# Kernel optimization log

Measured on AMD Instinct MI355X. Metric: run time of the kernel, lower is better.

Reference implementation:

```python
import jax, jax.numpy as jnp
import numpy as np

B, S, D = 2, 2048, 4096
NH, NKV = 32, 8
HD = D // NH  # 128
N_REP = NH // NKV  # 4


def setup_inputs() -> dict:
    key = jax.random.key(0)
    ks = jax.random.split(key, 5)
    scale = 0.02
    return {
        "x": jax.random.normal(ks[0], (B, S, D), dtype=jnp.float32),
        "wq": jax.random.normal(ks[1], (D, NH * HD), dtype=jnp.float32) * scale,
        "wk": jax.random.normal(ks[2], (D, NKV * HD), dtype=jnp.float32) * scale,
        "wv": jax.random.normal(ks[3], (D, NKV * HD), dtype=jnp.float32) * scale,
        "wo": jax.random.normal(ks[4], (NH * HD, D), dtype=jnp.float32) * scale,
    }


def reference(x, wq, wk, wv, wo):
    bsz, toks, _ = x.shape
    q = (x @ wq).reshape(bsz, toks, NH, HD)      # [B,S,NH,HD]
    k = (x @ wk).reshape(bsz, toks, NKV, HD)     # [B,S,NKV,HD]
    v = (x @ wv).reshape(bsz, toks, NKV, HD)
    # GQA: fold n_rep into einsum instead of materializing repeated K/V.
    qg = q.reshape(bsz, toks, NKV, N_REP, HD)    # group query heads per kv head
    scores = jnp.einsum('bqgrd,bkgd->bgrqk', qg, k) / jnp.sqrt(jnp.asarray(HD, x.dtype))
    attn = jax.nn.softmax(scores.astype(jnp.float32), axis=-1).astype(x.dtype)
    out = jnp.einsum('bgrqk,bkgd->bqgrd', attn, v)  # [B,S,NKV,N_REP,HD]
    out = out.reshape(bsz, toks, NH * HD)
    return out @ wo
```

## Files before the change

### kernel.cpp

```cpp
#include <hip/hip_runtime.h>
#include <math.h>

typedef _Float16 f16;
using f16x8 = __attribute__((ext_vector_type(8))) _Float16;
using f32x4 = __attribute__((ext_vector_type(4))) float;

#define BATCH 2
#define SEQ   2048
#define DMODEL 4096
#define NH    32
#define NKV   8
#define HD    128
#define MTOK  (BATCH*SEQ)

__global__ __launch_bounds__(256) void prep1_k(const float* __restrict__ x, f16* __restrict__ xh,
                                               const float* __restrict__ wq, f16* __restrict__ wqT,
                                               float scale) {
  __shared__ float tile[32][33];
  const int bid = blockIdx.x, t = threadIdx.x;
  if (bid < 8192) {
    const int i = bid * 256 + t;
    const float4* p = reinterpret_cast<const float4*>(x) + (size_t)i * 2;
    float4 a = p[0], b = p[1];
    f16x8 o = { (f16)a.x, (f16)a.y, (f16)a.z, (f16)a.w,
                (f16)b.x, (f16)b.y, (f16)b.z, (f16)b.w };
    reinterpret_cast<f16x8*>(xh)[i] = o;
  } else {
    const int bb = bid - 8192;
    const int n0 = (bb & 127) * 32, k0 = (bb >> 7) * 32;
    const int r = t >> 3, c4 = (t & 7) << 2;
    const float4 v = *reinterpret_cast<const float4*>(wq + (size_t)(k0 + r) * DMODEL + n0 + c4);
    tile[r][c4 + 0] = v.x; tile[r][c4 + 1] = v.y; tile[r][c4 + 2] = v.z; tile[r][c4 + 3] = v.w;
    __syncthreads();
    union { f16 h[4]; ushort4 u4; } pk;
    pk.h[0] = (f16)(tile[c4 + 0][r] * scale);
    pk.h[1] = (f16)(tile[c4 + 1][r] * scale);
    pk.h[2] = (f16)(tile[c4 + 2][r] * scale);
    pk.h[3] = (f16)(tile[c4 + 3][r] * scale);
    *reinterpret_cast<ushort4*>(wqT + (size_t)(n0 + r) * DMODEL + k0 + c4) = pk.u4;
  }
}

__global__ __launch_bounds__(256) void transpose_cvt_k(const float* __restrict__ w,
                                                       f16* __restrict__ wt, int Kd, int Nd,
                                                       float scale) {
  __shared__ float tile[32][33];
  const int t = threadIdx.x;
  const int n0 = blockIdx.x * 32, k0 = blockIdx.y * 32;
  const int r = t >> 3, c4 = (t & 7) << 2;
  const float4 v = *reinterpret_cast<const float4*>(w + (size_t)(k0 + r) * Nd + n0 + c4);
  tile[r][c4 + 0] = v.x; tile[r][c4 + 1] = v.y; tile[r][c4 + 2] = v.z; tile[r][c4 + 3] = v.w;
  __syncthreads();
  union { f16 h[4]; ushort4 u4; } pk;
  pk.h[0] = (f16)(tile[c4 + 0][r] * scale);
  pk.h[1] = (f16)(tile[c4 + 1][r] * scale);
  pk.h[2] = (f16)(tile[c4 + 2][r] * scale);
  pk.h[3] = (f16)(tile[c4 + 3][r] * scale);
  *reinterpret_cast<ushort4*>(wt + (size_t)(n0 + r) * Kd + k0 + c4) = pk.u4;
}

__global__ __launch_bounds__(256) void transpose_cvt2_k(const float* __restrict__ w0,
                                                        const float* __restrict__ w1,
                                                        f16* __restrict__ wt, int Kd, int Nd) {
  __shared__ float tile[32][33];
  const float* w = blockIdx.z ? w1 : w0;
  f16* dst = wt + (size_t)blockIdx.z * Nd * Kd;
  const int t = threadIdx.x;
  const int n0 = blockIdx.x * 32, k0 = blockIdx.y * 32;
  const int r = t >> 3, c4 = (t & 7) << 2;
  const float4 v = *reinterpret_cast<const float4*>(w + (size_t)(k0 + r) * Nd + n0 + c4);
  tile[r][c4 + 0] = v.x; tile[r][c4 + 1] = v.y; tile[r][c4 + 2] = v.z; tile[r][c4 + 3] = v.w;
  __syncthreads();
  union { f16 h[4]; ushort4 u4; } pk;
  pk.h[0] = (f16)tile[c4 + 0][r];
  pk.h[1] = (f16)tile[c4 + 1][r];
  pk.h[2] = (f16)tile[c4 + 2][r];
  pk.h[3] = (f16)tile[c4 + 3][r];
  *reinterpret_cast<ushort4*>(dst + (size_t)(n0 + r) * Kd + k0 + c4) = pk.u4;
}

__global__ __launch_bounds__(512, 2) void gemm_kv8_k(const f16* __restrict__ A,
                                                     const f16* __restrict__ BT,
                                                     f16* __restrict__ Kc,
                                                     f16* __restrict__ Vt,
                                                     int M, int N, int K) {
  __shared__ f16 lds[2 * 24576];
  char* ldsb = (char*)lds;

  const int t = threadIdx.x, lane = t & 63, w = t >> 6;
  const int wm = w >> 2, wn = w & 3;
  const int ll = lane & 15, lg = lane >> 4;
  const int nbn = N >> 8;
  const int nwg = gridDim.x, cpx = nwg >> 3, bid = blockIdx.x;
  const int swz = (bid & 7) * cpx + (bid >> 3);
  const int bm = swz / nbn, bn = swz % nbn;
  const size_t m0 = (size_t)bm << 7, n0 = (size_t)bn << 8;
  const int NT = K >> 6;

  const int uoff[4] = {0, 8192, 16384, 32768};

  auto stage = [&](int bufI, int unit, int ktS) {
    char* dstb = ldsb + (size_t)bufI * 49152 + uoff[unit];
    if (unit < 2) {
      const f16* base = A + (m0 + (size_t)(unit & 1) * 64) * (size_t)K;
      const int row = t >> 3, lin = t & 7;
      const int slot = lin ^ (row & 7);
      const f16* src = base + (size_t)row * K + ktS + slot * 8;
      __builtin_amdgcn_global_load_lds((const __attribute__((address_space(1))) void*)src,
          (__attribute__((address_space(3))) void*)(dstb + (size_t)t * 16), 16, 0, 0);
    } else {
      const f16* base = BT + (n0 + (size_t)(unit & 1) * 128) * (size_t)K;
#pragma unroll
      for (int rr = 0; rr < 2; rr++) {
        const int u = t + rr * 512;
        const int row = u >> 3, lin = u & 7;
        const int slot = lin ^ (row & 7);
        const f16* src = base + (size_t)row * K + ktS + slot * 8;
        __builtin_amdgcn_global_load_lds((const __attribute__((address_space(1))) void*)src,
            (__attribute__((address_space(3))) void*)(dstb + (size_t)u * 16), 16, 0, 0);
      }
    }
  };

  f32x4 acc[4][4];
#pragma unroll
  for (int i = 0; i < 4; i++)
#pragma unroll
    for (int j = 0; j < 4; j++) acc[i][j] = f32x4{0.f, 0.f, 0.f, 0.f};

  f16x8 af[2][2];
  f16x8 bfr[2][2][2];

  stage(0, 0, 0); stage(0, 1, 0); stage(0, 2, 0); stage(0, 3, 0);
  stage(1, 0, 64); stage(1, 2, 64); stage(1, 3, 64);
  asm volatile("s_waitcnt vmcnt(5)" ::: "memory");
  __builtin_amdgcn_sched_barrier(0);
  __builtin_amdgcn_s_barrier();

#define PHK(RBUF, RDA, RDB, SBUF, SUNIT, STILE, VM, MH, NHQ) do {                         \
    if ((RDA) >= 0) {                                                                     \
      const char* ab = ldsb + (size_t)(RBUF) * 49152 + uoff[MH];                          \
      _Pragma("unroll") for (int mi2 = 0; mi2 < 2; mi2++)                                 \
        _Pragma("unroll") for (int kk = 0; kk < 2; kk++) {                                \
          const int ri = wm * 32 + mi2 * 16 + ll;                                         \
          af[mi2][kk] = *reinterpret_cast<const f16x8*>(ab + ri * 128                     \
                               + ((((kk << 2) + lg) ^ (ri & 7)) << 4));                   \
        }                                                                                 \
    }                                                                                     \
    if ((RDB) >= 0) {                                                                     \
      const char* bb = ldsb + (size_t)(RBUF) * 49152 + uoff[2 + (RDB)];                   \
      _Pragma("unroll") for (int ni2 = 0; ni2 < 2; ni2++)                                 \
        _Pragma("unroll") for (int kk = 0; kk < 2; kk++) {                                \
          const int ri = wn * 32 + ni2 * 16 + ll;                                         \
          bfr[RDB][ni2][kk] = *reinterpret_cast<const f16x8*>(bb + ri * 128               \
                               + ((((kk << 2) + lg) ^ (ri & 7)) << 4));                   \
        }                                                                                 \
    }                                                                                     \
    stage((SBUF), (SUNIT), ((STILE) & (NT - 1)) << 6);                                    \
    if (VM) { asm volatile("s_waitcnt vmcnt(5)" ::: "memory");                            \
              __builtin_amdgcn_sched_barrier(0); }                                        \
    __builtin_amdgcn_s_barrier();                                                         \
    asm volatile("s_waitcnt lgkmcnt(0)" ::: "memory");                                    \
    __builtin_amdgcn_sched_barrier(0);                                                    \
    __builtin_amdgcn_s_setprio(1);                                                        \
    _Pragma("unroll") for (int kk = 0; kk < 2; kk++)                                      \
      _Pragma("unroll") for (int mi2 = 0; mi2 < 2; mi2++)                                 \
        _Pragma("unroll") for (int ni2 = 0; ni2 < 2; ni2++)                               \
          acc[(MH) * 2 + mi2][(NHQ) * 2 + ni2] = __builtin_amdgcn_mfma_f32_16x16x32_f16(  \
              af[mi2][kk], bfr[NHQ][ni2][kk], acc[(MH) * 2 + mi2][(NHQ) * 2 + ni2],       \
              0, 0, 0);                                                                   \
    __builtin_amdgcn_s_setprio(0);                                                        \
    __builtin_amdgcn_s_barrier();                                                         \
  } while (0)

  for (int tt = 0; tt < NT; tt += 2) {
    PHK(0,  0,  0, 1, 1, tt + 1, false, 0, 0);
    PHK(0, -1,  1, 0, 0, tt + 2, false, 0, 1);
    PHK(0,  1, -1, 0, 2, tt + 2, false, 1, 0);
    PHK(0, -1, -1, 0, 3, tt + 2, true , 1, 1);
    PHK(1,  0,  0, 0, 1, tt + 2, false, 0, 0);
    PHK(1, -1,  1, 1, 0, tt + 3, false, 0, 1);
    PHK(1,  1, -1, 1, 2, tt + 3, false, 1, 0);
    PHK(1, -1, -1, 1, 3, tt + 3, true , 1, 1);
  }
#undef PHK

#pragma unroll
  for (int mh = 0; mh < 2; mh++)
#pragma unroll
    for (int mi2 = 0; mi2 < 2; mi2++) {
      const size_t r0 = m0 + mh * 64 + wm * 32 + mi2 * 16 + lg * 4;
#pragma unroll
      for (int nh = 0; nh < 2; nh++)
#pragma unroll
        for (int ni2 = 0; ni2 < 2; ni2++) {
          const size_t c = n0 + nh * 128 + wn * 32 + ni2 * 16 + ll;
          const f32x4 v = acc[mh * 2 + mi2][nh * 2 + ni2];
          if ((int)c < 1024) {
#pragma unroll
            for (int rr = 0; rr < 4; rr++) Kc[(r0 + rr) * 1024 + c] = (f16)v[rr];
          } else {
            const int nc = (int)c - 1024;
            const int kvh = nc >> 7, d = nc & 127;
            const int b = (int)(r0 >> 11), sc = (int)(r0 & 2047);
            union { f16 h[4]; ushort4 u4; } pk;
#pragma unroll
            for (int rr = 0; rr < 4; rr++) pk.h[rr] = (f16)v[rr];
            *reinterpret_cast<ushort4*>(Vt + (((size_t)(b * NKV + kvh) * HD + d) * SEQ + sc)) = pk.u4;
          }
        }
    }
}

template<int MODE>
__global__ __launch_bounds__(512, 2) void gemm256_k(const f16* __restrict__ A,
                                                    const f16* __restrict__ BT,
                                                    void* __restrict__ Cv,
                                                    int M, int N, int K) {
  __shared__ f16 lds[2 * 4 * 128 * 64];
  char* ldsb = (char*)lds;

  const int t = threadIdx.x, lane = t & 63, w = t >> 6;
  const int wm = w >> 2, wn = w & 3;
  const int ll = lane & 15, lg = lane >> 4;
  const int nbn = N >> 8;
  const int nwg = gridDim.x, cpx = nwg >> 3, bid = blockIdx.x;
  const int swz = (bid & 7) * cpx + (bid >> 3);
  const int bm = swz / nbn, bn = swz % nbn;
  const size_t m0 = (size_t)bm << 8, n0 = (size_t)bn << 8;
  const int NT = K >> 6;

  auto stage = [&](int bufI, int unit, int ktS) {
    const f16* base = (unit < 2) ? (A + (m0 + (size_t)(unit & 1) * 128) * (size_t)K)
                                 : (BT + (n0 + (size_t)(unit & 1) * 128) * (size_t)K);
#pragma unroll
    for (int rr = 0; rr < 2; rr++) {
      const int u = t + rr * 512;
      const int row = u >> 3, lin = u & 7;
      const int slot = lin ^ (row & 7);
      const f16* src = base + (size_t)row * K + ktS + slot * 8;
      char* dst = ldsb + (size_t)(bufI * 4 + unit) * 16384 + (size_t)(w * 64 + rr * 512) * 16;
      __builtin_amdgcn_global_load_lds((const __attribute__((address_space(1))) void*)src,
          (__attribute__((address_space(3))) void*)dst, 16, 0, 0);
    }
  };

  f32x4 acc[8][4];
#pragma unroll
  for (int i = 0; i < 8; i++)
#pragma unroll
    for (int j = 0; j < 4; j++) acc[i][j] = f32x4{0.f, 0.f, 0.f, 0.f};

  f16x8 af[4][2];
  f16x8 bfr[2][2][2];

  stage(0, 0, 0); stage(0, 2, 0); stage(0, 3, 0); stage(0, 1, 0);
  stage(1, 0, 64); stage(1, 2, 64); stage(1, 3, 64);
  asm volatile("s_waitcnt vmcnt(6)" ::: "memory");
  __builtin_amdgcn_sched_barrier(0);
  __builtin_amdgcn_s_barrier();

#define PH(RBUF, RDA, RDB, SBUF, SUNIT, STILE, VM, MH, NHQ) do {                          \
    if ((RDA) >= 0) {                                                                     \
      const char* ab = ldsb + (size_t)((RBUF) * 4 + (RDA)) * 16384;                       \
      _Pragma("unroll") for (int mi = 0; mi < 4; mi++)                                    \
        _Pragma("unroll") for (int kk = 0; kk < 2; kk++)                                  \
          af[mi][kk] = *reinterpret_cast<const f16x8*>(ab + (mi * 32 + wm * 16 + ll) * 128\
                               + ((((kk << 2) + lg) ^ (ll & 7)) << 4));                   \
    }                                                                                     \
    if ((RDB) >= 0) {                                                                     \
      const char* bb = ldsb + (size_t)((RBUF) * 4 + 2 + (RDB)) * 16384;                   \
      _Pragma("unroll") for (int ni = 0; ni < 2; ni++)                                    \
        _Pragma("unroll") for (int kk = 0; kk < 2; kk++)                                  \
          bfr[RDB][ni][kk] = *reinterpret_cast<const f16x8*>(bb +                         \
                               (wn * 32 + ni * 16 + ll) * 128                             \
                               + ((((kk << 2) + lg) ^ (ll & 7)) << 4));                   \
    }                                                                                     \
    stage((SBUF), (SUNIT), ((STILE) & (NT - 1)) << 6);                                    \
    if (VM) { asm volatile("s_waitcnt vmcnt(6)" ::: "memory");                            \
              __builtin_amdgcn_sched_barrier(0); }                                        \
    __builtin_amdgcn_s_barrier();                                                         \
    asm volatile("s_waitcnt lgkmcnt(0)" ::: "memory");                                    \
    __builtin_amdgcn_sched_barrier(0);                                                    \
    __builtin_amdgcn_s_setprio(1);                                                        \
    _Pragma("unroll") for (int kk = 0; kk < 2; kk++)                                      \
      _Pragma("unroll") for (int mi = 0; mi < 4; mi++)                                    \
        _Pragma("unroll") for (int ni = 0; ni < 2; ni++)                                  \
          acc[(MH) * 4 + mi][(NHQ) * 2 + ni] = __builtin_amdgcn_mfma_f32_16x16x32_f16(    \
              af[mi][kk], bfr[NHQ][ni][kk], acc[(MH) * 4 + mi][(NHQ) * 2 + ni], 0, 0, 0); \
    __builtin_amdgcn_s_setprio(0);                                                        \
    __builtin_amdgcn_s_barrier();                                                         \
  } while (0)

  for (int tt = 0; tt < NT; tt += 2) {
    PH(0,  0,  0, 1, 1, tt + 1, false, 0, 0);
    PH(0, -1,  1, 0, 0, tt + 2, false, 0, 1);
    PH(0,  1, -1, 0, 2, tt + 2, false, 1, 0);
    PH(0, -1, -1, 0, 3, tt + 2, true , 1, 1);
    PH(1,  0,  0, 0, 1, tt + 2, false, 0, 0);
    PH(1, -1,  1, 1, 0, tt + 3, false, 0, 1);
    PH(1,  1, -1, 1, 2, tt + 3, false, 1, 0);
    PH(1, -1, -1, 1, 3, tt + 3, true , 1, 1);
  }
#undef PH

#pragma unroll
  for (int mh = 0; mh < 2; mh++)
#pragma unroll
    for (int mi = 0; mi < 4; mi++) {
      const size_t r0 = m0 + mh * 128 + mi * 32 + wm * 16 + lg * 4;
#pragma unroll
      for (int nh = 0; nh < 2; nh++)
#pragma unroll
        for (int ni = 0; ni < 2; ni++) {
          const size_t c = n0 + nh * 128 + wn * 32 + ni * 16 + ll;
          const f32x4 v = acc[mh * 4 + mi][nh * 2 + ni];
          if (MODE == 0) {
            f16* C = (f16*)Cv;
#pragma unroll
            for (int rr = 0; rr < 4; rr++) C[(r0 + rr) * N + c] = (f16)v[rr];
          } else {
            float* C = (float*)Cv;
#pragma unroll
            for (int rr = 0; rr < 4; rr++) C[(r0 + rr) * N + c] = v[rr];
          }
        }
    }
}

__global__ __launch_bounds__(512) void attn_k10(const f16* __restrict__ Q,
                                                const f16* __restrict__ Kb,
                                                const f16* __restrict__ VT,
                                                f16* __restrict__ ctx) {
  __shared__ f16 Klds[2][64 * 128];
  __shared__ f16 Vlds[2][128 * 64];
  __shared__ f16 Plds[8][16 * 64];

  const int t = threadIdx.x, lane = t & 63, w = t >> 6;
  const int bid = blockIdx.x;
  const int swz = (bid & 7) * 128 + (bid >> 3);
  const int qt = swz & 63, kvh = (swz >> 6) & 7, b = swz >> 9;
  const int h = kvh * 4 + (w & 3);
  const int q0 = qt * 32 + (w >> 2) * 16;
  const int ll = lane & 15, lg = lane >> 4;

  const f16* Qb = Q + ((size_t)(b * SEQ + q0) * NH + h) * HD;
  const f16* Kh = Kb + ((size_t)b * SEQ * NKV + kvh) * HD;
  const f16* Vh = VT + ((size_t)(b * NKV + kvh)) * HD * SEQ;

  f16x8 qf[4];
#pragma unroll
  for (int kd = 0; kd < 4; kd++)
    qf[kd] = *reinterpret_cast<const f16x8*>(Qb + (size_t)ll * (NH * HD) + kd * 32 + lg * 8);

  float m_ = -INFINITY;
  float l_ = 0.f;
  f32x4 o[8];
#pragma unroll
  for (int df = 0; df < 8; df++) o[df] = f32x4{0.f, 0.f, 0.f, 0.f};

  const float THR = 11.5416f;

  auto stage = [&](int bufi, int kt) {
#pragma unroll
    for (int rr = 0; rr < 2; rr++) {
      const int u = w * 128 + rr * 64 + lane;
      const int krow = u >> 4, klin = u & 15;
      const int kslot = klin ^ (krow & 7);
      const f16* ksrc = Kh + (size_t)(kt + krow) * (NKV * HD) + kslot * 8;
      __builtin_amdgcn_global_load_lds((const __attribute__((address_space(1))) void*)ksrc,
          (__attribute__((address_space(3))) void*)((char*)&Klds[bufi][0] + (size_t)u * 16), 16, 0, 0);
      const int vrow = u >> 3, vlin = u & 7;
      const int vslot = vlin ^ (vrow & 7);
      const f16* vsrc = Vh + (size_t)vrow * SEQ + kt + vslot * 8;
      __builtin_amdgcn_global_load_lds((const __attribute__((address_space(1))) void*)vsrc,
          (__attribute__((address_space(3))) void*)((char*)&Vlds[bufi][0] + (size_t)u * 16), 16, 0, 0);
    }
  };

  stage(0, 0);
  __syncthreads();

  for (int kt = 0; kt < SEQ; kt += 64) {
    const int buf = (kt >> 6) & 1;
    if (kt + 64 < SEQ) stage(buf ^ 1, kt + 64);

    const char* Kt = (const char*)Klds[buf];
    const char* Vt = (const char*)Vlds[buf];

    f32x4 s[4];
    __builtin_amdgcn_s_setprio(1);
#pragma unroll
    for (int nf = 0; nf < 4; nf++) {
      f32x4 a = f32x4{0.f, 0.f, 0.f, 0.f};
#pragma unroll
      for (int kd = 0; kd < 4; kd++) {
        const int row = nf * 16 + ll;
        f16x8 kf = *reinterpret_cast<const f16x8*>(
            Kt + row * 256 + ((((kd << 2) + lg) ^ (row & 7)) << 4));
        a = __builtin_amdgcn_mfma_f32_16x16x32_f16(kf, qf[kd], a, 0, 0, 0);
      }
      s[nf] = a;
    }
    __builtin_amdgcn_s_setprio(0);

    float mx = s[0][0];
#pragma unroll
    for (int nf = 0; nf < 4; nf++)
#pragma unroll
      for (int r = 0; r < 4; r++) mx = fmaxf(mx, s[nf][r]);

    if (!__all((int)(mx <= m_ + THR))) {
      float mr = fmaxf(mx, __shfl_xor(mx, 16, 64));
      mr = fmaxf(mr, __shfl_xor(mr, 32, 64));
      const float mn = fmaxf(m_, mr);
      const float corrq = __builtin_amdgcn_exp2f(m_ - mn);
      m_ = mn;
      l_ *= corrq;
#pragma unroll
      for (int r = 0; r < 4; r++) {
        const float c = __shfl(corrq, (lane & 48) | (lg * 4 + r), 64);
#pragma unroll
        for (int df = 0; df < 8; df++) o[df][r] *= c;
      }
    }

    float rs = 0.f;
#pragma unroll
    for (int nf = 0; nf < 4; nf++)
#pragma unroll
      for (int r = 0; r < 4; r++) {
        const float p = __builtin_amdgcn_exp2f(s[nf][r] - m_);
        s[nf][r] = p;
        rs += p;
      }
    rs += __shfl_xor(rs, 16, 64);
    rs += __shfl_xor(rs, 32, 64);
    l_ += rs;

    char* Pw = (char*)&Plds[w][0];
#pragma unroll
    for (int nf = 0; nf < 4; nf++) {
      union { f16 h[4]; ushort4 u4; } pk;
#pragma unroll
      for (int r = 0; r < 4; r++) pk.h[r] = (f16)s[nf][r];
      *reinterpret_cast<ushort4*>(Pw + ll * 128 + ((nf * 32 + lg * 8) ^ ((ll & 7) << 4))) = pk.u4;
    }

    f16x8 pf[2];
#pragma unroll
    for (int kf = 0; kf < 2; kf++)
      pf[kf] = *reinterpret_cast<const f16x8*>(Pw + ll * 128 + (((kf << 6) + (lg << 4)) ^ ((ll & 7) << 4)));

    __builtin_amdgcn_s_setprio(1);
#pragma unroll
    for (int kf = 0; kf < 2; kf++)
#pragma unroll
      for (int df = 0; df < 8; df++) {
        const int row = df * 16 + ll;
        f16x8 vf = *reinterpret_cast<const f16x8*>(
            Vt + row * 128 + ((((kf << 2) + lg) ^ (row & 7)) << 4));
        o[df] = __builtin_amdgcn_mfma_f32_16x16x32_f16(pf[kf], vf, o[df], 0, 0, 0);
      }
    __builtin_amdgcn_s_setprio(0);

    __syncthreads();
  }

  float inv[4];
#pragma unroll
  for (int r = 0; r < 4; r++) {
    const float lq = __shfl(l_, (lane & 48) | (lg * 4 + r), 64);
    inv[r] = 1.0f / lq;
  }
  f16* cb = ctx + ((size_t)(b * SEQ + q0) * NH + h) * HD;
#pragma unroll
  for (int df = 0; df < 8; df++)
#pragma unroll
    for (int r = 0; r < 4; r++)
      cb[(size_t)(lg * 4 + r) * (NH * HD) + df * 16 + ll] = (f16)(o[df][r] * inv[r]);
}

extern "C" void kernel_launch(void* const* d_in, const int* in_sizes, int n_in,
                              void* d_out, int out_size, void* d_ws, size_t ws_size,
                              hipStream_t stream) {
  (void)in_sizes; (void)n_in; (void)out_size;
  const float* x  = (const float*)d_in[0];
  const float* wq = (const float*)d_in[1];
  const float* wk = (const float*)d_in[2];
  const float* wv = (const float*)d_in[3];
  const float* wo = (const float*)d_in[4];
  float* out = (float*)d_out;

  const size_t SZ_X  = (size_t)MTOK * DMODEL * sizeof(f16);
  const size_t SZ_KV = (size_t)MTOK * NKV * HD * sizeof(f16);
  if (ws_size < 3 * SZ_X + 2 * SZ_KV) return;

  char* ws = (char*)d_ws;
  f16* xh  = (f16*)ws;
  f16* wT  = (f16*)(ws + SZ_X);
  f16* Qb  = (f16*)(ws + 2 * SZ_X);
  f16* Kb  = (f16*)(ws + 3 * SZ_X);
  f16* VTb = (f16*)(ws + 3 * SZ_X + SZ_KV);

  const float KSC2 = 0.08838834764831845f * 1.4426950408889634f;

  prep1_k<<<dim3(8192 + 16384), 256, 0, stream>>>(x, xh, wq, wT, KSC2);
  gemm256_k<0><<<dim3((MTOK / 256) * (DMODEL / 256)), 512, 0, stream>>>(xh, wT, Qb, MTOK, DMODEL, DMODEL);

  transpose_cvt2_k<<<dim3(NKV * HD / 32, DMODEL / 32, 2), 256, 0, stream>>>(wk, wv, wT, DMODEL, NKV * HD);
  gemm_kv8_k<<<dim3((MTOK / 128) * (2048 / 256)), 512, 0, stream>>>(xh, wT, Kb, VTb, MTOK, 2048, DMODEL);

  attn_k10<<<dim3(BATCH * NKV * (SEQ / 32)), 512, 0, stream>>>(Qb, Kb, VTb, xh);

  transpose_cvt_k<<<dim3(DMODEL / 32, DMODEL / 32), 256, 0, stream>>>(wo, wT, DMODEL, DMODEL, 1.0f);
  gemm256_k<2><<<dim3((MTOK / 256) * (DMODEL / 256)), 512, 0, stream>>>(xh, wT, out, MTOK, DMODEL, DMODEL);
}
```

Before: 526.3 us.

## Fuse all weight transposes into a single prep kernel with separate buffers

All weight conversion and transpose work (wq, wk, wv and optionally wo) now runs in one large prep launch, writing into separate workspace buffers when enough workspace is available. This removes three extra launches and the serial small transpose kernels between GEMMs. A fallback path keeps the old sequence when workspace is small. The gemm256 phase macro also gains a partial lgkmcnt wait before the barrier. The cost is extra workspace memory.

```diff
diff --git a/kernel.cpp b/kernel.cpp
--- a/kernel.cpp
+++ b/kernel.cpp
@@ -13,9 +13,12 @@
 #define HD    128
 #define MTOK  (BATCH*SEQ)
 
-__global__ __launch_bounds__(256) void prep1_k(const float* __restrict__ x, f16* __restrict__ xh,
-                                               const float* __restrict__ wq, f16* __restrict__ wqT,
-                                               float scale) {
+__global__ __launch_bounds__(256) void prep_k(const float* __restrict__ x, f16* __restrict__ xh,
+                                              const float* __restrict__ wq, f16* __restrict__ wqT,
+                                              const float* __restrict__ wk, const float* __restrict__ wv,
+                                              f16* __restrict__ wkvT,
+                                              const float* __restrict__ wo, f16* __restrict__ woT,
+                                              float scale) {
   __shared__ float tile[32][33];
   const int bid = blockIdx.x, t = threadIdx.x;
   if (bid < 8192) {
@@ -25,20 +28,26 @@
     f16x8 o = { (f16)a.x, (f16)a.y, (f16)a.z, (f16)a.w,
                 (f16)b.x, (f16)b.y, (f16)b.z, (f16)b.w };
     reinterpret_cast<f16x8*>(xh)[i] = o;
-  } else {
-    const int bb = bid - 8192;
-    const int n0 = (bb & 127) * 32, k0 = (bb >> 7) * 32;
-    const int r = t >> 3, c4 = (t & 7) << 2;
-    const float4 v = *reinterpret_cast<const float4*>(wq + (size_t)(k0 + r) * DMODEL + n0 + c4);
-    tile[r][c4 + 0] = v.x; tile[r][c4 + 1] = v.y; tile[r][c4 + 2] = v.z; tile[r][c4 + 3] = v.w;
-    __syncthreads();
-    union { f16 h[4]; ushort4 u4; } pk;
-    pk.h[0] = (f16)(tile[c4 + 0][r] * scale);
-    pk.h[1] = (f16)(tile[c4 + 1][r] * scale);
-    pk.h[2] = (f16)(tile[c4 + 2][r] * scale);
-    pk.h[3] = (f16)(tile[c4 + 3][r] * scale);
-    *reinterpret_cast<ushort4*>(wqT + (size_t)(n0 + r) * DMODEL + k0 + c4) = pk.u4;
+    return;
   }
+  const float* w; f16* dst; int Nd; float sc;
+  int bb;
+  if (bid < 24576)      { bb = bid - 8192;  w = wq; dst = wqT;  Nd = DMODEL; sc = scale; }
+  else if (bid < 32768) { bb = bid - 24576; const int z = bb >> 12; bb &= 4095;
+                          w = z ? wv : wk; dst = wkvT + (size_t)z * 1024 * DMODEL; Nd = 1024; sc = 1.0f; }
+  else                  { bb = bid - 32768; w = wo; dst = woT; Nd = DMODEL; sc = 1.0f; }
+  const int ntile = Nd >> 5;
+  const int n0 = (bb % ntile) * 32, k0 = (bb / ntile) * 32;
+  const int r = t >> 3, c4 = (t & 7) << 2;
+  const float4 v = *reinterpret_cast<const float4*>(w + (size_t)(k0 + r) * Nd + n0 + c4);
+  tile[r][c4 + 0] = v.x; tile[r][c4 + 1] = v.y; tile[r][c4 + 2] = v.z; tile[r][c4 + 3] = v.w;
+  __syncthreads();
+  union { f16 h[4]; ushort4 u4; } pk;
+  pk.h[0] = (f16)(tile[c4 + 0][r] * sc);
+  pk.h[1] = (f16)(tile[c4 + 1][r] * sc);
+  pk.h[2] = (f16)(tile[c4 + 2][r] * sc);
+  pk.h[3] = (f16)(tile[c4 + 3][r] * sc);
+  *reinterpret_cast<ushort4*>(dst + (size_t)(n0 + r) * DMODEL + k0 + c4) = pk.u4;
 }
 
 __global__ __launch_bounds__(256) void transpose_cvt_k(const float* __restrict__ w,
@@ -77,6 +86,17 @@
   pk.h[2] = (f16)tile[c4 + 2][r];
   pk.h[3] = (f16)tile[c4 + 3][r];
   *reinterpret_cast<ushort4*>(dst + (size_t)(n0 + r) * Kd + k0 + c4) = pk.u4;
+}
+
+__global__ __launch_bounds__(256) void cvt_f32_f16_k(const float* __restrict__ in,
+                                                     f16* __restrict__ out, int n8) {
+  int i = blockIdx.x * 256 + threadIdx.x;
+  if (i >= n8) return;
+  const float4* p = reinterpret_cast<const float4*>(in) + (size_t)i * 2;
+  float4 a = p[0], b = p[1];
+  f16x8 o = { (f16)a.x, (f16)a.y, (f16)a.z, (f16)a.w,
+              (f16)b.x, (f16)b.y, (f16)b.z, (f16)b.w };
+  reinterpret_cast<f16x8*>(out)[i] = o;
 }
 
 __global__ __launch_bounds__(512, 2) void gemm_kv8_k(const f16* __restrict__ A,
@@ -277,6 +297,8 @@
                                + ((((kk << 2) + lg) ^ (ll & 7)) << 4));                   \
     }                                                                                     \
     stage((SBUF), (SUNIT), ((STILE) & (NT - 1)) << 6);                                    \
+    if ((RDA) >= 0 && (RDB) >= 0)                                                         \
+      asm volatile("s_waitcnt lgkmcnt(8)" ::: "memory");     \
     if (VM) { asm volatile("s_waitcnt vmcnt(6)" ::: "memory");                            \
               __builtin_amdgcn_sched_barrier(0); }                                        \
     __builtin_amdgcn_s_barrier();                                                         \
@@ -328,7 +350,7 @@
     }
 }
 
-__global__ __launch_bounds__(512) void attn_k10(const f16* __restrict__ Q,
+__global__ __launch_bounds__(512) void attn_k11(const f16* __restrict__ Q,
                                                 const f16* __restrict__ Kb,
                                                 const f16* __restrict__ VT,
                                                 f16* __restrict__ ctx) {
@@ -492,27 +514,46 @@
   const float* wo = (const float*)d_in[4];
   float* out = (float*)d_out;
 
-  const size_t SZ_X  = (size_t)MTOK * DMODEL * sizeof(f16);
-  const size_t SZ_KV = (size_t)MTOK * NKV * HD * sizeof(f16);
-  if (ws_size < 3 * SZ_X + 2 * SZ_KV) return;
+  const size_t SZ_X   = (size_t)MTOK * DMODEL * sizeof(f16);
+  const size_t SZ_KV  = (size_t)MTOK * NKV * HD * sizeof(f16);
+  const size_t SZ_WKV = (size_t)2048 * DMODEL * sizeof(f16);
+  const size_t BASE   = 3 * SZ_X + 2 * SZ_KV;
+  if (ws_size < BASE) return;
 
   char* ws = (char*)d_ws;
-  f16* xh  = (f16*)ws;
-  f16* wT  = (f16*)(ws + SZ_X);
-  f16* Qb  = (f16*)(ws + 2 * SZ_X);
-  f16* Kb  = (f16*)(ws + 3 * SZ_X);
-  f16* VTb = (f16*)(ws + 3 * SZ_X + SZ_KV);
+  f16* xh   = (f16*)ws;
+  f16* wT   = (f16*)(ws + SZ_X);
+  f16* Qb   = (f16*)(ws + 2 * SZ_X);
+  f16* Kb   = (f16*)(ws + 3 * SZ_X);
+  f16* VTb  = (f16*)(ws + 3 * SZ_X + SZ_KV);
+  f16* wkvT = (f16*)(ws + BASE);
+  f16* woT  = (f16*)(ws + BASE + SZ_WKV);
 
   const float KSC2 = 0.08838834764831845f * 1.4426950408889634f;
 
-  prep1_k<<<dim3(8192 + 16384), 256, 0, stream>>>(x, xh, wq, wT, KSC2);
-  gemm256_k<0><<<dim3((MTOK / 256) * (DMODEL / 256)), 512, 0, stream>>>(xh, wT, Qb, MTOK, DMODEL, DMODEL);
-
-  transpose_cvt2_k<<<dim3(NKV * HD / 32, DMODEL / 32, 2), 256, 0, stream>>>(wk, wv, wT, DMODEL, NKV * HD);
-  gemm_kv8_k<<<dim3((MTOK / 128) * (2048 / 256)), 512, 0, stream>>>(xh, wT, Kb, VTb, MTOK, 2048, DMODEL);
-
-  attn_k10<<<dim3(BATCH * NKV * (SEQ / 32)), 512, 0, stream>>>(Qb, Kb, VTb, xh);
-
-  transpose_cvt_k<<<dim3(DMODEL / 32, DMODEL / 32), 256, 0, stream>>>(wo, wT, DMODEL, DMODEL, 1.0f);
-  gemm256_k<2><<<dim3((MTOK / 256) * (DMODEL / 256)), 512, 0, stream>>>(xh, wT, out, MTOK, DMODEL, DMODEL);
-}
+  const bool pathA = ws_size >= BASE + SZ_WKV + SZ_X;
+  const bool pathB = !pathA && ws_size >= BASE + SZ_WKV;
+
+  if (pathA || pathB) {
+    const int grid = pathA ? 49152 : 32768;
+    prep_k<<<dim3(grid), 256, 0, stream>>>(x, xh, wq, wT, wk, wv, wkvT, wo, woT, KSC2);
+    gemm256_k<0><<<dim3((MTOK / 256) * (DMODEL / 256)), 512, 0, stream>>>(xh, wT, Qb, MTOK, DMODEL, DMODEL);
+    gemm_kv8_k<<<dim3((MTOK / 128) * (2048 / 256)), 512, 0, stream>>>(xh, wkvT, Kb, VTb, MTOK, 2048, DMODEL);
+    attn_k11<<<dim3(BATCH * NKV * (SEQ / 32)), 512, 0, stream>>>(Qb, Kb, VTb, xh);
+    if (pathA) {
+      gemm256_k<2><<<dim3((MTOK / 256) * (DMODEL / 256)), 512, 0, stream>>>(xh, woT, out, MTOK, DMODEL, DMODEL);
+    } else {
+      transpose_cvt_k<<<dim3(DMODEL / 32, DMODEL / 32), 256, 0, stream>>>(wo, wT, DMODEL, DMODEL, 1.0f);
+      gemm256_k<2><<<dim3((MTOK / 256) * (DMODEL / 256)), 512, 0, stream>>>(xh, wT, out, MTOK, DMODEL, DMODEL);
+    }
+  } else {
+    cvt_f32_f16_k<<<dim3(MTOK * DMODEL / 8 / 256), 256, 0, stream>>>(x, xh, MTOK * DMODEL / 8);
+    transpose_cvt_k<<<dim3(DMODEL / 32, DMODEL / 32), 256, 0, stream>>>(wq, wT, DMODEL, DMODEL, KSC2);
+    gemm256_k<0><<<dim3((MTOK / 256) * (DMODEL / 256)), 512, 0, stream>>>(xh, wT, Qb, MTOK, DMODEL, DMODEL);
+    transpose_cvt2_k<<<dim3(NKV * HD / 32, DMODEL / 32, 2), 256, 0, stream>>>(wk, wv, wT, DMODEL, NKV * HD);
+    gemm_kv8_k<<<dim3((MTOK / 128) * (2048 / 256)), 512, 0, stream>>>(xh, wT, Kb, VTb, MTOK, 2048, DMODEL);
+    attn_k11<<<dim3(BATCH * NKV * (SEQ / 32)), 512, 0, stream>>>(Qb, Kb, VTb, xh);
+    transpose_cvt_k<<<dim3(DMODEL / 32, DMODEL / 32), 256, 0, stream>>>(wo, wT, DMODEL, DMODEL, 1.0f);
+    gemm256_k<2><<<dim3((MTOK / 256) * (DMODEL / 256)), 512, 0, stream>>>(xh, wT, out, MTOK, DMODEL, DMODEL);
+  }
+}
```

Measured after the change: 522.2 us. About the same (-0.8%).
